# Kernel tuning notes

Hardware: AMD Instinct MI355X
Metric: run time of the kernel (lower is better)

The kernel has to match this reference:

```python
import jax, jax.numpy as jnp
import numpy as np

N = 12288
IN_F = 128
OUT_F = 64
ALPHA = 0.2  # LeakyReLU negative slope
NEG_INF = -9e15


def setup_inputs() -> dict:
    key = jax.random.key(0)
    k1, k2, k3, k4 = jax.random.split(key, 4)
    input = jax.random.normal(k1, (N, IN_F), dtype=jnp.float32)
    adj = jax.random.randint(k2, (N, N), 0, 2, dtype=jnp.int32)
    # xavier-uniform-ish init with gain 1.414
    limW = 1.414 * np.sqrt(6.0 / (IN_F + OUT_F))
    W = jax.random.uniform(k3, (IN_F, OUT_F), dtype=jnp.float32, minval=-limW, maxval=limW)
    lima = 1.414 * np.sqrt(6.0 / (2 * OUT_F + 1))
    a = jax.random.uniform(k4, (2 * OUT_F, 1), dtype=jnp.float32, minval=-lima, maxval=lima)
    return {"input": input, "adj": adj, "W": W, "a": a}


def reference(input, adj, W, a):
    # h: (N, out_features)
    h = input @ W
    # broadcast attention logits: e[i,j] = leakyrelu(h_i . a1 + h_j . a2)
    Wh1 = h @ a[:OUT_F, :]          # (N, 1)
    Wh2 = h @ a[OUT_F:, :]          # (N, 1)
    e = Wh1 + Wh2.T                  # (N, N)
    e = jnp.where(e > 0, e, ALPHA * e)  # leaky relu
    # mask by adjacency, row softmax
    attention = jnp.where(adj > 0, e, NEG_INF)
    attention = jax.nn.softmax(attention, axis=1)
    # dropout is identity in eval mode (training=False)
    h_prime = attention @ h          # (N, out_features)
    return jax.nn.elu(h_prime)
```

## Files before the change

kernel.cpp:

```cpp
#include <hip/hip_runtime.h>

#define NN 12288
#define OUTF 64
#define ALPHA 0.2f
#define C1 6.0f
#define KSP 8
#define KRANGE (NN / KSP)
#define ITERS (KRANGE / 64)

typedef unsigned short u16;
typedef unsigned int u32;
typedef unsigned long long u64;
typedef _Float16 half8 __attribute__((ext_vector_type(8)));
typedef float floatx4 __attribute__((ext_vector_type(4)));
typedef int intx4 __attribute__((ext_vector_type(4)));

union H16 { u16 u; _Float16 h; };
__device__ __forceinline__ u16 f2h(float f) { H16 c; c.h = (_Float16)f; return c.u; }

__global__ __launch_bounds__(256) void k1_prep(
    const float* __restrict__ inp, const float* __restrict__ W, const float* __restrict__ a,
    u16* __restrict__ e1h, u16* __restrict__ thh,
    float* __restrict__ f1g, float* __restrict__ f2g, u16* __restrict__ Btf)
{
  __shared__ float Wl[128 * 64];
  __shared__ float hsm[16][66];
  __shared__ float e1sm[16], e2sm[16];
  const int tid = threadIdx.x;
  for (int t = tid; t < 128 * 64 / 4; t += 256)
    ((float4*)Wl)[t] = ((const float4*)W)[t];
  const int wave = tid >> 6, lane = tid & 63;
  const int k16 = blockIdx.x;
  const float a1l = a[lane], a2l = a[OUTF + lane];
  __syncthreads();
  for (int jl = 0; jl < 4; ++jl) {
    const int jn = wave * 4 + jl;
    const int j = k16 * 16 + jn;
    const float4* xp = (const float4*)(inp + (size_t)j * 128);
    float h = 0.f;
#pragma unroll
    for (int c4 = 0; c4 < 32; ++c4) {
      float4 v = xp[c4];
      const int k = c4 * 4;
      h += v.x * Wl[k * 64 + lane] + v.y * Wl[(k + 1) * 64 + lane]
         + v.z * Wl[(k + 2) * 64 + lane] + v.w * Wl[(k + 3) * 64 + lane];
    }
    float p1 = h * a1l, p2 = h * a2l;
#pragma unroll
    for (int off = 32; off > 0; off >>= 1) { p1 += __shfl_xor(p1, off); p2 += __shfl_xor(p2, off); }
    hsm[jn][lane] = h;
    if (lane == 0) {
      const float s1 = p1, s2 = p2;
      const float e1 = expf(s2 - C1), e2 = expf(ALPHA * s2);
      e1sm[jn] = e1; e2sm[jn] = e2;
      e1h[j] = f2h(e1);
      thh[j] = f2h(expf(-s1 - C1));
      f1g[j] = expf(s1 + C1);
      f2g[j] = expf(ALPHA * s1);
    }
  }
  __syncthreads();
  const int k32 = k16 >> 1, hi = (k16 & 1) * 32;
  for (int cc = tid; cc < 320; cc += 256) {
    const int n = cc >> 5, l32 = cc & 31;
    const int r = n * 16 + (l32 & 15);
    const int jb = (l32 >> 4) * 8;
    u32 wpk[4];
#pragma unroll
    for (int p = 0; p < 4; ++p) {
      u16 hh[2];
#pragma unroll
      for (int q2 = 0; q2 < 2; ++q2) {
        const int jj = jb + p * 2 + q2;
        float v;
        if (r < 64)        v = e1sm[jj] * hsm[jj][r];
        else if (r == 64)  v = e1sm[jj];
        else if (r < 80)   v = 0.f;
        else if (r < 144)  v = e2sm[jj] * hsm[jj][r - 80];
        else if (r == 144) v = e2sm[jj];
        else               v = 0.f;
        hh[q2] = f2h(v);
      }
      wpk[p] = (u32)hh[0] | ((u32)hh[1] << 16);
    }
    ((uint4*)Btf)[(size_t)(k32 * 10 + n) * 64 + hi + l32] = make_uint4(wpk[0], wpk[1], wpk[2], wpk[3]);
  }
}

__global__ __launch_bounds__(256) void k_pack(
    const int* __restrict__ adj, const u16* __restrict__ e1h, const u16* __restrict__ thh,
    unsigned char* __restrict__ P1, unsigned char* __restrict__ P2)
{
  const int i = blockIdx.x, tid = threadIdx.x;
  const u16 th = thh[i];
  const int* arow = adj + (size_t)i * NN;
  unsigned char* p1r = P1 + (size_t)i * (NN / 8);
  unsigned char* p2r = P2 + (size_t)i * (NN / 8);
#pragma unroll
  for (int it = 0; it < NN / 2048; ++it) {
    const int cb = it * 2048 + tid * 8;
    intx4 a0 = *reinterpret_cast<const intx4*>(arow + cb);
    intx4 a1 = *reinterpret_cast<const intx4*>(arow + cb + 4);
    uint4 ev = *reinterpret_cast<const uint4*>(e1h + cb);
    const int av[8] = {a0.x, a0.y, a0.z, a0.w, a1.x, a1.y, a1.z, a1.w};
    const u32 ew[4] = {ev.x, ev.y, ev.z, ev.w};
    u32 b1 = 0, b2 = 0;
#pragma unroll
    for (int e = 0; e < 8; ++e) {
      const u16 eh = (u16)(ew[e >> 1] >> ((e & 1) * 16));
      const bool bit = av[e] != 0;
      const bool up = eh > th;
      b1 |= (u32)(bit && up) << e;
      b2 |= (u32)(bit && !up) << e;
    }
    p1r[it * 256 + tid] = (unsigned char)b1;
    p2r[it * 256 + tid] = (unsigned char)b2;
  }
}

__global__ __launch_bounds__(256, 3) void k2_main(
    const u64* __restrict__ P1, const u64* __restrict__ P2,
    const u16* __restrict__ Btf, float* __restrict__ part)
{
  __shared__ u16 sB[2][10240];
  const int tid = threadIdx.x;
  const int wave = tid >> 6, lane = tid & 63;
  const int quad = lane >> 4, lr = lane & 15;
  const int mpos = (int)blockIdx.x >> 3;
  const int ks = (int)blockIdx.x & 7;
  const int mbase = mpos * 128 + wave * 32;
  const int k0 = ks * KRANGE;

  const u64* p1r[2] = {P1 + (size_t)(mbase + lr) * 192, P1 + (size_t)(mbase + 16 + lr) * 192};
  const u64* p2r[2] = {P2 + (size_t)(mbase + lr) * 192, P2 + (size_t)(mbase + 16 + lr) * 192};

  floatx4 acc[2][10];
#pragma unroll
  for (int t = 0; t < 2; ++t)
#pragma unroll
    for (int n = 0; n < 10; ++n) acc[t][n] = (floatx4){0.f, 0.f, 0.f, 0.f};

  const uint4* gB = (const uint4*)Btf;
  {
    const uint4* src = gB + (size_t)(k0 >> 5) * 640;
#pragma unroll
    for (int i = 0; i < 5; ++i) ((uint4*)sB[0])[tid + i * 256] = src[tid + i * 256];
  }

  u64 P1w[2], P2w[2];
  for (int it = 0; it < ITERS; ++it) {
    __syncthreads();
    const int cur = it & 1;
    uint4 stg[5];
    const bool more = (it + 1 < ITERS);
    if (more) {
      const uint4* src = gB + (size_t)((k0 + (it + 1) * 64) >> 5) * 640;
#pragma unroll
      for (int i = 0; i < 5; ++i) stg[i] = src[tid + i * 256];
    }
    if ((it & 3) == 0) {
      const int kw0 = (k0 >> 6) + it;
#pragma unroll
      for (int t = 0; t < 2; ++t) {
        P1w[t] = p1r[t][kw0 + quad];
        P2w[t] = p2r[t][kw0 + quad];
      }
    }
    const int j = it & 3;
    u64 b1[2], b2[2];
#pragma unroll
    for (int t = 0; t < 2; ++t) {
      b1[t] = __shfl(P1w[t], (j << 4) | lr);
      b2[t] = __shfl(P2w[t], (j << 4) | lr);
    }
#pragma unroll
    for (int h = 0; h < 2; ++h) {
      const u32 sh = (u32)(h * 32 + quad * 8);
      union { half8 v; u16 s[8]; } A1[2], A2[2];
      const u32 m1a = (u32)(b1[0] >> sh) & 0xFFu, m2a = (u32)(b2[0] >> sh) & 0xFFu;
      const u32 m1b = (u32)(b1[1] >> sh) & 0xFFu, m2b = (u32)(b2[1] >> sh) & 0xFFu;
#pragma unroll
      for (int e = 0; e < 8; ++e) {
        A1[0].s[e] = ((m1a >> e) & 1u) ? (u16)0x3C00 : (u16)0;
        A2[0].s[e] = ((m2a >> e) & 1u) ? (u16)0x3C00 : (u16)0;
        A1[1].s[e] = ((m1b >> e) & 1u) ? (u16)0x3C00 : (u16)0;
        A2[1].s[e] = ((m2b >> e) & 1u) ? (u16)0x3C00 : (u16)0;
      }
      const u16* bp = &sB[cur][h * 5120];
#pragma unroll
      for (int n = 0; n < 10; ++n) {
        half8 Bv = *(const half8*)(bp + (n * 64 + lane) * 8);
        acc[0][n] = __builtin_amdgcn_mfma_f32_16x16x32_f16(n < 5 ? A1[0].v : A2[0].v, Bv,
                                                           acc[0][n], 0, 0, 0);
        acc[1][n] = __builtin_amdgcn_mfma_f32_16x16x32_f16(n < 5 ? A1[1].v : A2[1].v, Bv,
                                                           acc[1][n], 0, 0, 0);
      }
    }
    if (more) {
      const int nb = cur ^ 1;
#pragma unroll
      for (int i = 0; i < 5; ++i) ((uint4*)sB[nb])[tid + i * 256] = stg[i];
    }
  }

  const int ks96 = ks * 96 + mpos;
#pragma unroll
  for (int t = 0; t < 2; ++t) {
    float* pp = part + ((size_t)ks96 * 128 + wave * 32 + t * 16 + quad * 4) * 132;
#pragma unroll
    for (int r = 0; r < 4; ++r) {
#pragma unroll
      for (int n = 0; n < 4; ++n)
        pp[r * 132 + n * 16 + lr] = acc[t][n][r];
#pragma unroll
      for (int n = 5; n < 9; ++n)
        pp[r * 132 + 64 + (n - 5) * 16 + lr] = acc[t][n][r];
      if (lr == 0) {
        pp[r * 132 + 128] = acc[t][4][r];
        pp[r * 132 + 129] = acc[t][9][r];
      }
    }
  }
}

__global__ __launch_bounds__(256) void k3_final(
    const float* __restrict__ part, const float* __restrict__ f1g,
    const float* __restrict__ f2g, float* __restrict__ out)
{
  const int gid = blockIdx.x * 256 + threadIdx.x;
  const int row = gid >> 6, col = gid & 63;
  const int mpos = row >> 7, r = row & 127;
  float n1 = 0.f, n2 = 0.f, d1 = 0.f, d2 = 0.f;
#pragma unroll
  for (int ks = 0; ks < KSP; ++ks) {
    const float* p = part + ((size_t)(ks * 96 + mpos) * 128 + r) * 132;
    n1 += p[col]; n2 += p[64 + col]; d1 += p[128]; d2 += p[129];
  }
  const float f1 = f1g[row], f2 = f2g[row];
  const float num = f1 * n1 + f2 * n2;
  const float den = fmaxf(f1 * d1 + f2 * d2, 1e-30f);
  const float x = num / den;
  out[gid] = x > 0.f ? x : (expf(x) - 1.f);
}

extern "C" void kernel_launch(void* const* d_in, const int* in_sizes, int n_in,
                              void* d_out, int out_size, void* d_ws, size_t ws_size,
                              hipStream_t stream) {
  const float* inp = (const float*)d_in[0];
  const int* adj = (const int*)d_in[1];
  const float* W = (const float*)d_in[2];
  const float* a = (const float*)d_in[3];

  char* ws = (char*)d_ws;
  u16* Btf = (u16*)ws;
  unsigned char* P1 = (unsigned char*)(ws + 3932160);
  unsigned char* P2 = P1 + 18874368;
  float* part = (float*)(ws + 3932160 + 2 * 18874368);
  char* tail = ws + 3932160 + 2 * 18874368 + 51904512;
  u16* e1h = (u16*)tail;
  u16* thh = e1h + NN;
  float* f1g = (float*)(thh + NN);
  float* f2g = f1g + NN;

  k1_prep<<<768, 256, 0, stream>>>(inp, W, a, e1h, thh, f1g, f2g, Btf);
  k_pack<<<NN, 256, 0, stream>>>(adj, e1h, thh, P1, P2);
  k2_main<<<768, 256, 0, stream>>>((const u64*)P1, (const u64*)P2, Btf, part);
  k3_final<<<NN * OUTF / 256, 256, 0, stream>>>(part, f1g, f2g, (float*)d_out);
}
```

Baseline: 898.8 us.

## Fuse adjacency bit-packing into main MFMA kernel with direct global-to-LDS loads

Removes the separate k_pack kernel and the round trip through global memory for the P1/P2 bitmasks. Each k2_main block now reads its int32 adjacency tile and e1h values, builds the two masks, and keeps them double-buffered in shared memory. B-tile staging also moves from register staging to global_load_lds, which asynchronously copies global data straight into LDS. The adjacency read (about 600 MB) now sits inside the MFMA loop, so compute and streaming must overlap within one kernel. This adds register pressure and puts the mask computation on the critical path.

After: 850.6 us, median of 2. 5.4% less time.

```diff
diff --git a/kernel.cpp b/kernel.cpp
--- a/kernel.cpp
+++ b/kernel.cpp
@@ -17,6 +17,12 @@
 
 union H16 { u16 u; _Float16 h; };
 __device__ __forceinline__ u16 f2h(float f) { H16 c; c.h = (_Float16)f; return c.u; }
+
+__device__ __forceinline__ void g2l16(const void* g, void* l) {
+  __builtin_amdgcn_global_load_lds(
+      (const __attribute__((address_space(1))) void*)g,
+      (__attribute__((address_space(3))) void*)l, 16, 0, 0);
+}
 
 __global__ __launch_bounds__(256) void k1_prep(
     const float* __restrict__ inp, const float* __restrict__ W, const float* __restrict__ a,
@@ -87,52 +93,27 @@
   }
 }
 
-__global__ __launch_bounds__(256) void k_pack(
+__global__ __launch_bounds__(256, 3) void k2_main(
     const int* __restrict__ adj, const u16* __restrict__ e1h, const u16* __restrict__ thh,
-    unsigned char* __restrict__ P1, unsigned char* __restrict__ P2)
-{
-  const int i = blockIdx.x, tid = threadIdx.x;
-  const u16 th = thh[i];
-  const int* arow = adj + (size_t)i * NN;
-  unsigned char* p1r = P1 + (size_t)i * (NN / 8);
-  unsigned char* p2r = P2 + (size_t)i * (NN / 8);
-#pragma unroll
-  for (int it = 0; it < NN / 2048; ++it) {
-    const int cb = it * 2048 + tid * 8;
-    intx4 a0 = *reinterpret_cast<const intx4*>(arow + cb);
-    intx4 a1 = *reinterpret_cast<const intx4*>(arow + cb + 4);
-    uint4 ev = *reinterpret_cast<const uint4*>(e1h + cb);
-    const int av[8] = {a0.x, a0.y, a0.z, a0.w, a1.x, a1.y, a1.z, a1.w};
-    const u32 ew[4] = {ev.x, ev.y, ev.z, ev.w};
-    u32 b1 = 0, b2 = 0;
-#pragma unroll
-    for (int e = 0; e < 8; ++e) {
-      const u16 eh = (u16)(ew[e >> 1] >> ((e & 1) * 16));
-      const bool bit = av[e] != 0;
-      const bool up = eh > th;
-      b1 |= (u32)(bit && up) << e;
-      b2 |= (u32)(bit && !up) << e;
-    }
-    p1r[it * 256 + tid] = (unsigned char)b1;
-    p2r[it * 256 + tid] = (unsigned char)b2;
-  }
-}
-
-__global__ __launch_bounds__(256, 3) void k2_main(
-    const u64* __restrict__ P1, const u64* __restrict__ P2,
     const u16* __restrict__ Btf, float* __restrict__ part)
 {
   __shared__ u16 sB[2][10240];
+  __shared__ u64 m1s[2][128];
+  __shared__ u64 m2s[2][128];
   const int tid = threadIdx.x;
   const int wave = tid >> 6, lane = tid & 63;
   const int quad = lane >> 4, lr = lane & 15;
   const int mpos = (int)blockIdx.x >> 3;
   const int ks = (int)blockIdx.x & 7;
-  const int mbase = mpos * 128 + wave * 32;
+  const int mbase = mpos * 128;
   const int k0 = ks * KRANGE;
 
-  const u64* p1r[2] = {P1 + (size_t)(mbase + lr) * 192, P1 + (size_t)(mbase + 16 + lr) * 192};
-  const u64* p2r[2] = {P2 + (size_t)(mbase + lr) * 192, P2 + (size_t)(mbase + 16 + lr) * 192};
+  const int prow = tid >> 3, pcol = tid & 7;
+  u16 thu[4];
+#pragma unroll
+  for (int p = 0; p < 4; ++p) thu[p] = thh[mbase + p * 32 + prow];
+  const int* aB = adj + (size_t)(mbase + prow) * NN + k0 + pcol * 8;
+  const u16* eB = e1h + k0 + pcol * 8;
 
   floatx4 acc[2][10];
 #pragma unroll
@@ -140,45 +121,66 @@
 #pragma unroll
     for (int n = 0; n < 10; ++n) acc[t][n] = (floatx4){0.f, 0.f, 0.f, 0.f};
 
-  const uint4* gB = (const uint4*)Btf;
+  intx4 aj[4][2];
+  uint4 evv;
+
   {
-    const uint4* src = gB + (size_t)(k0 >> 5) * 640;
-#pragma unroll
-    for (int i = 0; i < 5; ++i) ((uint4*)sB[0])[tid + i * 256] = src[tid + i * 256];
-  }
-
-  u64 P1w[2], P2w[2];
+    const char* src = (const char*)(Btf + ((size_t)(k0 >> 5)) * 5120);
+#pragma unroll
+    for (int i = 0; i < 5; ++i)
+      g2l16(src + i * 4096 + tid * 16, (char*)&sB[0][0] + i * 4096 + wave * 1024);
+#pragma unroll
+    for (int p = 0; p < 4; ++p) {
+      aj[p][0] = __builtin_nontemporal_load((const intx4*)(aB + (size_t)p * 32 * NN));
+      aj[p][1] = __builtin_nontemporal_load((const intx4*)(aB + (size_t)p * 32 * NN + 4));
+    }
+    evv = *(const uint4*)eB;
+    u32 ev8[8] = {evv.x & 0xFFFFu, evv.x >> 16, evv.y & 0xFFFFu, evv.y >> 16,
+                  evv.z & 0xFFFFu, evv.z >> 16, evv.w & 0xFFFFu, evv.w >> 16};
+#pragma unroll
+    for (int p = 0; p < 4; ++p) {
+      const int av[8] = {aj[p][0].x, aj[p][0].y, aj[p][0].z, aj[p][0].w,
+                         aj[p][1].x, aj[p][1].y, aj[p][1].z, aj[p][1].w};
+      u32 b1 = 0, b2 = 0;
+#pragma unroll
+      for (int e = 0; e < 8; ++e) {
+        const bool nbr = av[e] > 0;
+        const bool up = ev8[e] > (u32)thu[p];
+        b1 |= (u32)(nbr && up) << e;
+        b2 |= (u32)(nbr && !up) << e;
+      }
+      ((unsigned char*)&m1s[0][p * 32 + prow])[pcol] = (unsigned char)b1;
+      ((unsigned char*)&m2s[0][p * 32 + prow])[pcol] = (unsigned char)b2;
+    }
+  }
+
   for (int it = 0; it < ITERS; ++it) {
     __syncthreads();
-    const int cur = it & 1;
-    uint4 stg[5];
+    const int cur = it & 1, nxt = cur ^ 1;
     const bool more = (it + 1 < ITERS);
     if (more) {
-      const uint4* src = gB + (size_t)((k0 + (it + 1) * 64) >> 5) * 640;
-#pragma unroll
-      for (int i = 0; i < 5; ++i) stg[i] = src[tid + i * 256];
-    }
-    if ((it & 3) == 0) {
-      const int kw0 = (k0 >> 6) + it;
-#pragma unroll
-      for (int t = 0; t < 2; ++t) {
-        P1w[t] = p1r[t][kw0 + quad];
-        P2w[t] = p2r[t][kw0 + quad];
-      }
-    }
-    const int j = it & 3;
-    u64 b1[2], b2[2];
-#pragma unroll
-    for (int t = 0; t < 2; ++t) {
-      b1[t] = __shfl(P1w[t], (j << 4) | lr);
-      b2[t] = __shfl(P2w[t], (j << 4) | lr);
-    }
+      const char* src = (const char*)(Btf + ((size_t)(k0 >> 5) + (it + 1) * 2) * 5120);
+#pragma unroll
+      for (int i = 0; i < 5; ++i)
+        g2l16(src + i * 4096 + tid * 16, (char*)&sB[nxt][0] + i * 4096 + wave * 1024);
+      const int koff = (it + 1) * 64;
+#pragma unroll
+      for (int p = 0; p < 4; ++p) {
+        aj[p][0] = __builtin_nontemporal_load((const intx4*)(aB + (size_t)p * 32 * NN + koff));
+        aj[p][1] = __builtin_nontemporal_load((const intx4*)(aB + (size_t)p * 32 * NN + koff + 4));
+      }
+      evv = *(const uint4*)(eB + koff);
+    }
+
+    u64 w1[2], w2[2];
+    w1[0] = m1s[cur][wave * 32 + lr];      w1[1] = m1s[cur][wave * 32 + 16 + lr];
+    w2[0] = m2s[cur][wave * 32 + lr];      w2[1] = m2s[cur][wave * 32 + 16 + lr];
 #pragma unroll
     for (int h = 0; h < 2; ++h) {
       const u32 sh = (u32)(h * 32 + quad * 8);
       union { half8 v; u16 s[8]; } A1[2], A2[2];
-      const u32 m1a = (u32)(b1[0] >> sh) & 0xFFu, m2a = (u32)(b2[0] >> sh) & 0xFFu;
-      const u32 m1b = (u32)(b1[1] >> sh) & 0xFFu, m2b = (u32)(b2[1] >> sh) & 0xFFu;
+      const u32 m1a = (u32)(w1[0] >> sh) & 0xFFu, m2a = (u32)(w2[0] >> sh) & 0xFFu;
+      const u32 m1b = (u32)(w1[1] >> sh) & 0xFFu, m2b = (u32)(w2[1] >> sh) & 0xFFu;
 #pragma unroll
       for (int e = 0; e < 8; ++e) {
         A1[0].s[e] = ((m1a >> e) & 1u) ? (u16)0x3C00 : (u16)0;
@@ -196,10 +198,25 @@
                                                            acc[1][n], 0, 0, 0);
       }
     }
+
     if (more) {
-      const int nb = cur ^ 1;
-#pragma unroll
-      for (int i = 0; i < 5; ++i) ((uint4*)sB[nb])[tid + i * 256] = stg[i];
+      u32 ev8[8] = {evv.x & 0xFFFFu, evv.x >> 16, evv.y & 0xFFFFu, evv.y >> 16,
+                    evv.z & 0xFFFFu, evv.z >> 16, evv.w & 0xFFFFu, evv.w >> 16};
+#pragma unroll
+      for (int p = 0; p < 4; ++p) {
+        const int av[8] = {aj[p][0].x, aj[p][0].y, aj[p][0].z, aj[p][0].w,
+                           aj[p][1].x, aj[p][1].y, aj[p][1].z, aj[p][1].w};
+        u32 b1 = 0, b2 = 0;
+#pragma unroll
+        for (int e = 0; e < 8; ++e) {
+          const bool nbr = av[e] > 0;
+          const bool up = ev8[e] > (u32)thu[p];
+          b1 |= (u32)(nbr && up) << e;
+          b2 |= (u32)(nbr && !up) << e;
+        }
+        ((unsigned char*)&m1s[nxt][p * 32 + prow])[pcol] = (unsigned char)b1;
+        ((unsigned char*)&m2s[nxt][p * 32 + prow])[pcol] = (unsigned char)b2;
+      }
     }
   }
 
@@ -253,17 +270,14 @@
 
   char* ws = (char*)d_ws;
   u16* Btf = (u16*)ws;
-  unsigned char* P1 = (unsigned char*)(ws + 3932160);
-  unsigned char* P2 = P1 + 18874368;
-  float* part = (float*)(ws + 3932160 + 2 * 18874368);
-  char* tail = ws + 3932160 + 2 * 18874368 + 51904512;
+  float* part = (float*)(ws + 3932160);
+  char* tail = ws + 3932160 + 51904512;
   u16* e1h = (u16*)tail;
   u16* thh = e1h + NN;
   float* f1g = (float*)(thh + NN);
   float* f2g = f1g + NN;
 
   k1_prep<<<768, 256, 0, stream>>>(inp, W, a, e1h, thh, f1g, f2g, Btf);
-  k_pack<<<NN, 256, 0, stream>>>(adj, e1h, thh, P1, P2);
-  k2_main<<<768, 256, 0, stream>>>((const u64*)P1, (const u64*)P2, Btf, part);
+  k2_main<<<768, 256, 0, stream>>>(adj, e1h, thh, Btf, part);
   k3_final<<<NN * OUTF / 256, 256, 0, stream>>>(part, f1g, f2g, (float*)d_out);
 }
```
